# Kernel optimization log

Measured on AMD Instinct MI355X. Metric: run time of the kernel, lower is better.

## Reference

```python
import jax, jax.numpy as jnp
import numpy as np
from jax import lax

HEADS = 8
L, B, D, H, V, T = 128, 16, 512, 512, 16000, 32


def setup_inputs() -> dict:
    key = jax.random.key(0)
    ks = jax.random.split(key, 16)
    p = lambda k, shape, fan: (jax.random.normal(k, shape, jnp.float32) * (fan ** -0.5))
    output_len = jnp.sort(jax.random.randint(ks[15], (B,), 1, T + 1))[::-1]
    output_len = output_len.at[0].set(T)  # max(output_len) == T, sorted descending
    return dict(
        memory=jax.random.normal(ks[0], (L, B, D), jnp.float32),
        emb=p(ks[1], (V, H), H),
        Wq=p(ks[2], (2 * H, H), 2 * H), bq=jnp.zeros((H,), jnp.float32),
        Wk=p(ks[3], (D, H), D), bk=jnp.zeros((H,), jnp.float32),
        Wv=p(ks[4], (D, H), D), bv=jnp.zeros((H,), jnp.float32),
        W_ih=p(ks[5], (H, 3 * H), H), b_ih=p(ks[6], (3 * H,), H),
        W_hh=p(ks[7], (H, 3 * H), H), b_hh=p(ks[8], (3 * H,), H),
        Wf=p(ks[9], (H, V), H), bf=jnp.zeros((V,), jnp.float32),
        output_len=output_len.astype(jnp.int32),
        max_output_len=T,
    )


def _forward(memory, emb, Wq, bq, Wk, bk, Wv, bv, W_ih, b_ih, W_hh, b_hh, Wf, bf,
             output_len, max_output_len):
    Lm, bs, _ = memory.shape
    Hh = emb.shape[1]
    dk = Hh // HEADS
    scale = 1.0 / np.sqrt(dk)

    def mha(query):  # query: (1, bs, 2H); recomputes k/v projections each step (faithful)
        qh = (query @ Wq + bq).reshape(1, bs, HEADS, dk).transpose(2, 1, 0, 3)   # (h,b,1,dk)
        kh = (memory @ Wk + bk).reshape(Lm, bs, HEADS, dk).transpose(2, 1, 0, 3)  # (h,b,L,dk)
        vh = (memory @ Wv + bv).reshape(Lm, bs, HEADS, dk).transpose(2, 1, 0, 3)
        score = jax.nn.softmax(jnp.einsum('hbqd,hbkd->hbqk', qh, kh) * scale, axis=-1)
        ctx = jnp.einsum('hbqk,hbkd->hbqd', score, vh)          # (h,b,1,dk)
        ctx = ctx.transpose(2, 1, 0, 3).reshape(1, bs, Hh)       # (1,b,H)
        sc = score.transpose(2, 1, 0, 3).mean(axis=2)            # (1,b,L) mean over heads
        return ctx, sc

    def gru_cell(x, h):  # (bs,H),(bs,H) -> (bs,H); PyTorch GRU equations
        gi = x @ W_ih + b_ih
        gh = h @ W_hh + b_hh
        ir, iz, inn = jnp.split(gi, 3, axis=-1)
        hr, hz, hn = jnp.split(gh, 3, axis=-1)
        r = jax.nn.sigmoid(ir + hr)
        z = jax.nn.sigmoid(iz + hz)
        n = jnp.tanh(inn + r * hn)
        return (1.0 - z) * n + z * h

    def step(carry, i):
        out, hid = carry  # (bs,V), (bs,H)
        embedded = emb[jnp.argmax(out, axis=-1)]                 # (bs,H)
        query = jnp.concatenate([embedded, hid], axis=-1)[None]  # (1,bs,2H)
        ctx, sc = mha(query)
        h_new = gru_cell(ctx[0], hid)
        logits = h_new @ Wf + bf                                 # fc on GRU output
        # masking replaces torch's shrinking-batch slicing (output_len sorted desc)
        active = (i < output_len)[:, None].astype(logits.dtype)
        return (logits, h_new), (logits * active, h_new * active, sc[0] * active)

    init = (jnp.zeros((bs, Wf.shape[1]), memory.dtype), jnp.zeros((bs, Hh), memory.dtype))
    _, (outputs, hiddens, scores) = lax.scan(step, init, jnp.arange(max_output_len))
    return outputs, hiddens, scores


def reference(memory, emb, Wq, bq, Wk, bk, Wv, bv, W_ih, b_ih, W_hh, b_hh, Wf, bf,
              output_len, max_output_len):
    return _forward(memory, emb, Wq, bq, Wk, bk, Wv, bv, W_ih, b_ih, W_hh, b_hh,
                    Wf, bf, output_len, max_output_len)
```

## Files before the change

### kernel.cpp

```cpp
#include <hip/hip_runtime.h>

#define LL 128
#define BB 16
#define HH 512
#define VV 16000
#define TT 32
#define NH 8
#define DK 64

#define WS_K 0
#define WS_V (LL*BB*HH)
#define WS_HID0 (2*LL*BB*HH)
#define WS_HID1 (WS_HID0 + BB*HH)
#define WS_CTX  (WS_HID1 + BB*HH)
#define WS_P    (WS_CTX + BB*HH)
#define WS_HS   (WS_P + BB*NH*LL)
#define WS_SLOTS_F (WS_HS + 6*BB*HH)

#define OUT_HID_OFF ((size_t)TT*BB*VV)
#define OUT_SC_OFF  (OUT_HID_OFF + (size_t)TT*BB*HH)


__global__ __launch_bounds__(256) void kv_kernel(const float* __restrict__ mem,
        const float* __restrict__ Wk, const float* __restrict__ bk,
        const float* __restrict__ Wv, const float* __restrict__ bv,
        float* __restrict__ ws) {
    int blk = blockIdx.x;
    int rg = blk >> 4, ct = blk & 15;
    int isV = ct >= 8;
    int colbase = (ct & 7) * 64;
    const float* W = isV ? Wv : Wk;
    const float* bias = isV ? bv : bk;
    float* outp = ws + (isV ? WS_V : WS_K);
    int rowbase = rg * 16;
    int tid = threadIdx.x;
    __shared__ float As[16*516];

    {
        const float4* srcp = (const float4*)(mem + (size_t)rowbase*512);
        #pragma unroll
        for (int j = 0; j < 8; ++j) {
            int i = tid + 256*j;
            float4 v = srcp[i];
            int row = i >> 7, c4i = i & 127;
            *(float4*)(As + row*516 + c4i*4) = v;
        }
    }
    if (blk == 0) {
        for (int i = tid; i < BB*HH; i += 256) ws[WS_HID0 + i] = 0.f;
        unsigned long long* slots = (unsigned long long*)(ws + WS_SLOTS_F);
        for (int i = tid; i < (TT+1)*BB; i += 256)
            slots[i] = (i < BB) ? 0xFFFFFFFFull : 0ull;
    }
    __syncthreads();

    int cq = tid & 15;
    int rq4 = (tid >> 4) & 3;
    int kq = tid >> 6;
    float acc[4][4];
    #pragma unroll
    for (int i = 0; i < 4; ++i) { acc[i][0]=0.f; acc[i][1]=0.f; acc[i][2]=0.f; acc[i][3]=0.f; }
    const float* wp = W + colbase + cq*4;
    for (int k4 = kq*32; k4 < kq*32 + 32; ++k4) {
        float4 a0 = *(const float4*)(As + (rq4*4+0)*516 + k4*4);
        float4 a1 = *(const float4*)(As + (rq4*4+1)*516 + k4*4);
        float4 a2 = *(const float4*)(As + (rq4*4+2)*516 + k4*4);
        float4 a3 = *(const float4*)(As + (rq4*4+3)*516 + k4*4);
        const float* wrow = wp + (size_t)(4*k4)*512;
        float4 w0 = *(const float4*)(wrow);
        float4 w1 = *(const float4*)(wrow + 512);
        float4 w2 = *(const float4*)(wrow + 1024);
        float4 w3 = *(const float4*)(wrow + 1536);
        #define KV_FMA(ri, A) \
            acc[ri][0] += A.x*w0.x + A.y*w1.x + A.z*w2.x + A.w*w3.x; \
            acc[ri][1] += A.x*w0.y + A.y*w1.y + A.z*w2.y + A.w*w3.y; \
            acc[ri][2] += A.x*w0.z + A.y*w1.z + A.z*w2.z + A.w*w3.z; \
            acc[ri][3] += A.x*w0.w + A.y*w1.w + A.z*w2.w + A.w*w3.w;
        KV_FMA(0, a0) KV_FMA(1, a1) KV_FMA(2, a2) KV_FMA(3, a3)
        #undef KV_FMA
    }
    __syncthreads();
    float* red = As;
    #pragma unroll
    for (int ri = 0; ri < 4; ++ri)
        *(float4*)(red + ri*1024 + tid*4) =
            make_float4(acc[ri][0], acc[ri][1], acc[ri][2], acc[ri][3]);
    __syncthreads();
    {
        int c4 = tid & 15, row = tid >> 4;
        int rq = row >> 2, ri = row & 3;
        float4 b4v = *(const float4*)(bias + colbase + c4*4);
        float o[4] = {b4v.x, b4v.y, b4v.z, b4v.w};
        #pragma unroll
        for (int kq2 = 0; kq2 < 4; ++kq2) {
            const float* pr = red + ri*1024 + (kq2*64 + rq*16 + c4)*4;
            o[0] += pr[0]; o[1] += pr[1]; o[2] += pr[2]; o[3] += pr[3];
        }
        *(float4*)(outp + (size_t)(rowbase + row)*512 + colbase + c4*4) =
            make_float4(o[0], o[1], o[2], o[3]);
    }
}

__global__ __launch_bounds__(256) void attn_kernel(
        const float* __restrict__ emb, const float* __restrict__ Wq,
        const float* __restrict__ bq, float* __restrict__ ws, int t) {
    int b = blockIdx.x >> 3, h = blockIdx.x & 7;
    int tid = threadIdx.x;
    const float* hid = ws + ((t & 1) ? WS_HID1 : WS_HID0);
    unsigned long long* slots = (unsigned long long*)(ws + WS_SLOTS_F);
    __shared__ float q[2*HH];
    __shared__ float part[8*64];
    __shared__ float qh[64];
    __shared__ float sp[2*LL];
    __shared__ float p[LL];
    __shared__ float cpart[4*64];

    unsigned long long slot = slots[t*BB + b];
    unsigned idx = 0xFFFFFFFFu - (unsigned)(slot & 0xFFFFFFFFull);
    for (int i = tid; i < HH; i += 256) {
        q[i] = emb[(size_t)idx*HH + i];
        q[HH + i] = hid[b*HH + i];
    }
    __syncthreads();

    {
        int c2 = tid & 31, kc = tid >> 5;
        const float* wp = Wq + (size_t)(kc*128)*HH + h*64 + c2*2;
        const float* qp = q + kc*128;
        float a0 = 0.f, a1 = 0.f;
        #pragma unroll 8
        for (int kk = 0; kk < 128; ++kk) {
            float x = qp[kk];
            float2 w2 = *(const float2*)(wp + (size_t)kk*HH);
            a0 += x*w2.x; a1 += x*w2.y;
        }
        part[kc*64 + c2*2]     = a0;
        part[kc*64 + c2*2 + 1] = a1;
    }
    __syncthreads();
    if (tid < 64) {
        float s = bq[h*64 + tid];
        #pragma unroll
        for (int kc = 0; kc < 8; ++kc) s += part[kc*64 + tid];
        qh[tid] = s;
    }
    __syncthreads();

    {
        int l = tid & 127, jh = tid >> 7;
        const float4* kr = (const float4*)(ws + WS_K + ((size_t)(l*BB + b))*HH + h*DK) + jh*8;
        const float4* q4 = (const float4*)qh + jh*8;
        float acc = 0.f;
        #pragma unroll
        for (int j = 0; j < 8; ++j) {
            float4 kv = kr[j], qq = q4[j];
            acc += qq.x*kv.x + qq.y*kv.y + qq.z*kv.z + qq.w*kv.w;
        }
        sp[jh*128 + l] = acc;
    }
    __syncthreads();

    if (tid < 64) {
        float s0 = (sp[tid]      + sp[128 + tid]) * 0.125f;
        float s1 = (sp[64 + tid] + sp[192 + tid]) * 0.125f;
        float m = fmaxf(s0, s1);
        #pragma unroll
        for (int off = 32; off; off >>= 1) m = fmaxf(m, __shfl_xor(m, off));
        float e0 = expf(s0 - m), e1 = expf(s1 - m);
        float sum = e0 + e1;
        #pragma unroll
        for (int off = 32; off; off >>= 1) sum += __shfl_xor(sum, off);
        float inv = 1.f / sum;
        p[tid]      = e0 * inv;
        p[64 + tid] = e1 * inv;
    }
    __syncthreads();
    if (tid < 128) ws[WS_P + (size_t)(b*NH + h)*LL + tid] = p[tid];

    {
        int c = tid & 63, lc = tid >> 6;
        const float* Vp = ws + WS_V + h*DK + c;
        float acc = 0.f;
        #pragma unroll 8
        for (int li = 0; li < 32; ++li) {
            int l = lc*32 + li;
            acc += p[l] * Vp[(size_t)(l*BB + b)*HH];
        }
        cpart[lc*64 + c] = acc;
    }
    __syncthreads();
    if (tid < 64)
        ws[WS_CTX + b*HH + h*DK + tid] =
            cpart[tid] + cpart[64+tid] + cpart[128+tid] + cpart[192+tid];
}

__global__ __launch_bounds__(512) void gates_kernel(
        const float* __restrict__ Wih, const float* __restrict__ bih,
        const float* __restrict__ Whh, const float* __restrict__ bhh,
        const int* __restrict__ olen, float* __restrict__ ws,
        float* __restrict__ out, int t) {
    int cb = blockIdx.x;
    int tid = threadIdx.x;
    const float* hid_in = ws + ((t & 1) ? WS_HID1 : WS_HID0);
    float* hid_out = ws + ((t & 1) ? WS_HID0 : WS_HID1);
    const float* ctx = ws + WS_CTX;
    __shared__ float xs[512*20];
    __shared__ float hh[512*20];
    __shared__ float part[8*256];
    __shared__ float gacc[6*256];

    for (int i = tid; i < BB*HH; i += 512) {
        int bb = i >> 9, k = i & 511;
        xs[k*20 + bb] = ctx[i];
        hh[k*20 + bb] = hid_in[i];
    }
    if (tid < 64) {
        int e = cb*64 + tid;
        int b = e >> 7, l = e & 127;
        float s = 0.f;
        #pragma unroll
        for (int hq = 0; hq < NH; ++hq)
            s += ws[WS_P + (size_t)(b*NH + hq)*LL + l];
        out[OUT_SC_OFF + ((size_t)t*BB + b)*LL + l] = (t < olen[b]) ? s*0.125f : 0.f;
    }
    __syncthreads();

    int c4 = tid & 3, b4 = (tid >> 2) & 3, kc = tid >> 4;
    int wv = tid >> 6;
    for (int g = 0; g < 6; ++g) {
        const float* W = (g < 3) ? Wih : Whh;
        int gg = (g < 3) ? g : g - 3;
        const float* xsrc = (g < 3) ? xs : hh;
        const float* wp = W + (size_t)kc*(3*HH) + gg*HH + cb*16 + c4*4;
        const float* xp = xsrc + kc*20 + b4*4;
        float acc[4][4];
        #pragma unroll
        for (int i = 0; i < 4; ++i) { acc[i][0]=0.f; acc[i][1]=0.f; acc[i][2]=0.f; acc[i][3]=0.f; }
        #pragma unroll 8
        for (int i = 0; i < 16; ++i) {
            float4 w4 = *(const float4*)wp;
            float4 x4 = *(const float4*)xp;
            wp += (size_t)32*(3*HH);
            xp += 32*20;
            acc[0][0] += x4.x*w4.x; acc[0][1] += x4.x*w4.y; acc[0][2] += x4.x*w4.z; acc[0][3] += x4.x*w4.w;
            acc[1][0] += x4.y*w4.x; acc[1][1] += x4.y*w4.y; acc[1][2] += x4.y*w4.z; acc[1][3] += x4.y*w4.w;
            acc[2][0] += x4.z*w4.x; acc[2][1] += x4.z*w4.y; acc[2][2] += x4.z*w4.z; acc[2][3] += x4.z*w4.w;
            acc[3][0] += x4.w*w4.x; acc[3][1] += x4.w*w4.y; acc[3][2] += x4.w*w4.z; acc[3][3] += x4.w*w4.w;
        }
        #pragma unroll
        for (int bi = 0; bi < 4; ++bi)
            #pragma unroll
            for (int ci = 0; ci < 4; ++ci) {
                float v = acc[bi][ci];
                v += __shfl_xor(v, 16);
                v += __shfl_xor(v, 32);
                acc[bi][ci] = v;
            }
        if ((tid & 48) == 0) {
            #pragma unroll
            for (int bi = 0; bi < 4; ++bi)
                *(float4*)(part + wv*256 + (b4*4+bi)*16 + c4*4) =
                    make_float4(acc[bi][0], acc[bi][1], acc[bi][2], acc[bi][3]);
        }
        __syncthreads();
        if (tid < 256) {
            int b = tid >> 4, c = tid & 15;
            float s = 0.f;
            #pragma unroll
            for (int w = 0; w < 8; ++w) s += part[w*256 + b*16 + c];
            gacc[g*256 + b*16 + c] = s;
        }
        __syncthreads();
    }

    if (tid < 256) {
        int b = tid >> 4, c = tid & 15;
        int col = cb*16 + c;
        float gir = gacc[0*256 + b*16 + c] + bih[col];
        float giz = gacc[1*256 + b*16 + c] + bih[HH + col];
        float gin = gacc[2*256 + b*16 + c] + bih[2*HH + col];
        float ghr = gacc[3*256 + b*16 + c] + bhh[col];
        float ghz = gacc[4*256 + b*16 + c] + bhh[HH + col];
        float ghn = gacc[5*256 + b*16 + c] + bhh[2*HH + col];
        float r = 1.f/(1.f + __expf(-(gir + ghr)));
        float z = 1.f/(1.f + __expf(-(giz + ghz)));
        float xn = gin + r*ghn;
        float n = 1.f - 2.f/(__expf(2.f*xn) + 1.f);
        float hprev = hh[col*20 + b];
        float hnew = (1.f - z)*n + z*hprev;
        hid_out[b*HH + col] = hnew;
        out[OUT_HID_OFF + ((size_t)t*BB + b)*HH + col] = (t < olen[b]) ? hnew : 0.f;
        ws[WS_HS + col*16 + b] = hnew;
    }
}

__global__ __launch_bounds__(256) void logits_kernel(
        const float* __restrict__ Wf, const float* __restrict__ bf,
        const int* __restrict__ olen, float* __restrict__ ws,
        float* __restrict__ out, int t) {
    __shared__ float hs[HH*20];
    __shared__ float red[4*512];
    __shared__ unsigned long long am[BB*16];
    int tid = threadIdx.x;

    {
        const float4* s4 = (const float4*)(ws + WS_HS);
        #pragma unroll
        for (int j = 0; j < 8; ++j) {
            int i = tid + 256*j;
            float4 v = s4[i];
            int row = i >> 2, qo = i & 3;
            *(float4*)(hs + row*20 + qo*4) = v;
        }
    }
    __syncthreads();

    int c4 = tid & 7, kc = tid >> 3;
    int colbase = blockIdx.x * 32;
    float acc[16][4];
    #pragma unroll
    for (int bi = 0; bi < 16; ++bi) { acc[bi][0]=0.f; acc[bi][1]=0.f; acc[bi][2]=0.f; acc[bi][3]=0.f; }
    const float* wp = Wf + (size_t)kc*VV + colbase + c4*4;
    const float* hp = hs + kc*20;
    #pragma unroll 8
    for (int i = 0; i < 16; ++i) {
        float4 w4 = *(const float4*)wp;
        float4 h0 = *(const float4*)(hp);
        float4 h1 = *(const float4*)(hp + 4);
        float4 h2 = *(const float4*)(hp + 8);
        float4 h3 = *(const float4*)(hp + 12);
        wp += (size_t)32 * VV;
        hp += 32 * 20;
        #define LACC(bi, hv) acc[bi][0] += (hv)*w4.x; acc[bi][1] += (hv)*w4.y; \
                             acc[bi][2] += (hv)*w4.z; acc[bi][3] += (hv)*w4.w;
        LACC(0,h0.x)  LACC(1,h0.y)  LACC(2,h0.z)  LACC(3,h0.w)
        LACC(4,h1.x)  LACC(5,h1.y)  LACC(6,h1.z)  LACC(7,h1.w)
        LACC(8,h2.x)  LACC(9,h2.y)  LACC(10,h2.z) LACC(11,h2.w)
        LACC(12,h3.x) LACC(13,h3.y) LACC(14,h3.z) LACC(15,h3.w)
        #undef LACC
    }

    #pragma unroll
    for (int bi = 0; bi < 16; ++bi)
        #pragma unroll
        for (int ci = 0; ci < 4; ++ci) {
            float v = acc[bi][ci];
            v += __shfl_xor(v, 8);
            v += __shfl_xor(v, 16);
            v += __shfl_xor(v, 32);
            acc[bi][ci] = v;
        }
    int wv = tid >> 6;
    if ((tid & 56) == 0) {
        #pragma unroll
        for (int bi = 0; bi < 16; ++bi)
            *(float4*)(red + wv*512 + bi*32 + c4*4) =
                make_float4(acc[bi][0], acc[bi][1], acc[bi][2], acc[bi][3]);
    }
    __syncthreads();

    {
        int b = tid >> 4, cp = (tid & 15) * 2;
        float2 bf2 = *(const float2*)(bf + colbase + cp);
        float v0 = bf2.x, v1 = bf2.y;
        #pragma unroll
        for (int w = 0; w < 4; ++w) {
            v0 += red[w*512 + b*32 + cp];
            v1 += red[w*512 + b*32 + cp + 1];
        }
        bool active = t < olen[b];
        float2 ov; ov.x = active ? v0 : 0.f; ov.y = active ? v1 : 0.f;
        *(float2*)(out + ((size_t)t*BB + b)*VV + colbase + cp) = ov;

        unsigned u0 = __float_as_uint(v0);
        u0 = (u0 & 0x80000000u) ? ~u0 : (u0 | 0x80000000u);
        unsigned u1 = __float_as_uint(v1);
        u1 = (u1 & 0x80000000u) ? ~u1 : (u1 | 0x80000000u);
        unsigned long long e0 = ((unsigned long long)u0 << 32)
                              | (unsigned long long)(0xFFFFFFFFu - (unsigned)(colbase + cp));
        unsigned long long e1 = ((unsigned long long)u1 << 32)
                              | (unsigned long long)(0xFFFFFFFFu - (unsigned)(colbase + cp + 1));
        am[b*16 + (tid & 15)] = e0 > e1 ? e0 : e1;
    }
    __syncthreads();
    if (tid < BB) {
        unsigned long long m = 0ull;
        #pragma unroll
        for (int i = 0; i < 16; ++i) {
            unsigned long long v = am[tid*16 + i];
            m = v > m ? v : m;
        }
        unsigned long long* slots = (unsigned long long*)(ws + WS_SLOTS_F);
        atomicMax(&slots[(size_t)(t+1)*BB + tid], m);
    }
}

extern "C" void kernel_launch(void* const* d_in, const int* in_sizes, int n_in,
                              void* d_out, int out_size, void* d_ws, size_t ws_size,
                              hipStream_t stream) {
    const float* mem = (const float*)d_in[0];
    const float* emb = (const float*)d_in[1];
    const float* Wq  = (const float*)d_in[2];
    const float* bq  = (const float*)d_in[3];
    const float* Wk  = (const float*)d_in[4];
    const float* bk  = (const float*)d_in[5];
    const float* Wv  = (const float*)d_in[6];
    const float* bv  = (const float*)d_in[7];
    const float* Wih = (const float*)d_in[8];
    const float* bih = (const float*)d_in[9];
    const float* Whh = (const float*)d_in[10];
    const float* bhh = (const float*)d_in[11];
    const float* Wf  = (const float*)d_in[12];
    const float* bf  = (const float*)d_in[13];
    const int* olen  = (const int*)d_in[14];
    float* out = (float*)d_out;
    float* ws  = (float*)d_ws;

    hipLaunchKernelGGL(kv_kernel, dim3(2048), dim3(256), 0, stream, mem, Wk, bk, Wv, bv, ws);
    for (int t = 0; t < TT; ++t) {
        hipLaunchKernelGGL(attn_kernel, dim3(BB*NH), dim3(256), 0, stream, emb, Wq, bq, ws, t);
        hipLaunchKernelGGL(gates_kernel, dim3(32), dim3(512), 0, stream,
                           Wih, bih, Whh, bhh, olen, ws, out, t);
        hipLaunchKernelGGL(logits_kernel, dim3(500), dim3(256), 0, stream,
                           Wf, bf, olen, ws, out, t);
    }
}
```

Measured before the change: 1.463 ms.

## Fuse per-step kernels into persistent mega kernel with software grid barriers

Replaces the 96 per-timestep launches of the attention, gate and logits kernels with one persistent kernel of 250 blocks of 512 threads. The stages are separated by an atomic sense-reversing grid barrier, which removes launch overhead and inter-kernel gaps. Hidden state and context are kept in transposed layout so the GRU can read the hidden state directly from global memory. Each stage is re-tiled for 512 threads, and logits now use 64 columns per block across 250 blocks. The cost is that stages run on fewer blocks, and correctness relies on all 250 blocks being co-resident, with deadlock possible otherwise.

```diff
diff --git a/kernel.cpp b/kernel.cpp
--- a/kernel.cpp
+++ b/kernel.cpp
@@ -7,15 +7,16 @@
 #define TT 32
 #define NH 8
 #define DK 64
+#define NBLK 250
 
 #define WS_K 0
 #define WS_V (LL*BB*HH)
-#define WS_HID0 (2*LL*BB*HH)
-#define WS_HID1 (WS_HID0 + BB*HH)
-#define WS_CTX  (WS_HID1 + BB*HH)
-#define WS_P    (WS_CTX + BB*HH)
-#define WS_HS   (WS_P + BB*NH*LL)
-#define WS_SLOTS_F (WS_HS + 6*BB*HH)
+#define WS_CTXT (2*LL*BB*HH)
+#define WS_HS0 (WS_CTXT + BB*HH)
+#define WS_HS1 (WS_HS0 + BB*HH)
+#define WS_P   (WS_HS1 + BB*HH)
+#define WS_SLOTS_F (WS_P + BB*NH*LL)
+#define WS_BAR (WS_SLOTS_F + 2*(TT+1)*BB + 16)
 
 #define OUT_HID_OFF ((size_t)TT*BB*VV)
 #define OUT_SC_OFF  (OUT_HID_OFF + (size_t)TT*BB*HH)
@@ -47,10 +48,11 @@
         }
     }
     if (blk == 0) {
-        for (int i = tid; i < BB*HH; i += 256) ws[WS_HID0 + i] = 0.f;
+        for (int i = tid; i < BB*HH; i += 256) ws[WS_HS0 + i] = 0.f;
         unsigned long long* slots = (unsigned long long*)(ws + WS_SLOTS_F);
         for (int i = tid; i < (TT+1)*BB; i += 256)
             slots[i] = (i < BB) ? 0xFFFFFFFFull : 0ull;
+        if (tid == 0) *(unsigned*)(ws + WS_BAR) = 0u;
     }
     __syncthreads();
 
@@ -101,297 +103,345 @@
     }
 }
 
-__global__ __launch_bounds__(256) void attn_kernel(
+__device__ __forceinline__ void gridbar(unsigned* cnt, unsigned* sense,
+                                        unsigned target) {
+    __syncthreads();
+    if (threadIdx.x == 0) {
+        __threadfence();
+        unsigned old = atomicAdd(cnt, 1u);
+        if (old == (unsigned)NBLK - 1u) {
+            __hip_atomic_store(cnt, 0u, __ATOMIC_RELAXED, __HIP_MEMORY_SCOPE_AGENT);
+            __hip_atomic_fetch_add(sense, 1u, __ATOMIC_RELEASE, __HIP_MEMORY_SCOPE_AGENT);
+        } else {
+            while ((int)(__hip_atomic_load(sense, __ATOMIC_RELAXED,
+                         __HIP_MEMORY_SCOPE_AGENT) - target) < 0)
+                __builtin_amdgcn_s_sleep(8);
+        }
+        __threadfence();
+    }
+    __syncthreads();
+}
+
+__global__ __launch_bounds__(512) void mega_kernel(
         const float* __restrict__ emb, const float* __restrict__ Wq,
-        const float* __restrict__ bq, float* __restrict__ ws, int t) {
-    int b = blockIdx.x >> 3, h = blockIdx.x & 7;
-    int tid = threadIdx.x;
-    const float* hid = ws + ((t & 1) ? WS_HID1 : WS_HID0);
-    unsigned long long* slots = (unsigned long long*)(ws + WS_SLOTS_F);
-    __shared__ float q[2*HH];
-    __shared__ float part[8*64];
-    __shared__ float qh[64];
-    __shared__ float sp[2*LL];
-    __shared__ float p[LL];
-    __shared__ float cpart[4*64];
-
-    unsigned long long slot = slots[t*BB + b];
-    unsigned idx = 0xFFFFFFFFu - (unsigned)(slot & 0xFFFFFFFFull);
-    for (int i = tid; i < HH; i += 256) {
-        q[i] = emb[(size_t)idx*HH + i];
-        q[HH + i] = hid[b*HH + i];
-    }
-    __syncthreads();
-
-    {
-        int c2 = tid & 31, kc = tid >> 5;
-        const float* wp = Wq + (size_t)(kc*128)*HH + h*64 + c2*2;
-        const float* qp = q + kc*128;
-        float a0 = 0.f, a1 = 0.f;
-        #pragma unroll 8
-        for (int kk = 0; kk < 128; ++kk) {
-            float x = qp[kk];
-            float2 w2 = *(const float2*)(wp + (size_t)kk*HH);
-            a0 += x*w2.x; a1 += x*w2.y;
-        }
-        part[kc*64 + c2*2]     = a0;
-        part[kc*64 + c2*2 + 1] = a1;
-    }
-    __syncthreads();
-    if (tid < 64) {
-        float s = bq[h*64 + tid];
-        #pragma unroll
-        for (int kc = 0; kc < 8; ++kc) s += part[kc*64 + tid];
-        qh[tid] = s;
-    }
-    __syncthreads();
-
-    {
-        int l = tid & 127, jh = tid >> 7;
-        const float4* kr = (const float4*)(ws + WS_K + ((size_t)(l*BB + b))*HH + h*DK) + jh*8;
-        const float4* q4 = (const float4*)qh + jh*8;
-        float acc = 0.f;
-        #pragma unroll
-        for (int j = 0; j < 8; ++j) {
-            float4 kv = kr[j], qq = q4[j];
-            acc += qq.x*kv.x + qq.y*kv.y + qq.z*kv.z + qq.w*kv.w;
-        }
-        sp[jh*128 + l] = acc;
-    }
-    __syncthreads();
-
-    if (tid < 64) {
-        float s0 = (sp[tid]      + sp[128 + tid]) * 0.125f;
-        float s1 = (sp[64 + tid] + sp[192 + tid]) * 0.125f;
-        float m = fmaxf(s0, s1);
-        #pragma unroll
-        for (int off = 32; off; off >>= 1) m = fmaxf(m, __shfl_xor(m, off));
-        float e0 = expf(s0 - m), e1 = expf(s1 - m);
-        float sum = e0 + e1;
-        #pragma unroll
-        for (int off = 32; off; off >>= 1) sum += __shfl_xor(sum, off);
-        float inv = 1.f / sum;
-        p[tid]      = e0 * inv;
-        p[64 + tid] = e1 * inv;
-    }
-    __syncthreads();
-    if (tid < 128) ws[WS_P + (size_t)(b*NH + h)*LL + tid] = p[tid];
-
-    {
-        int c = tid & 63, lc = tid >> 6;
-        const float* Vp = ws + WS_V + h*DK + c;
-        float acc = 0.f;
-        #pragma unroll 8
-        for (int li = 0; li < 32; ++li) {
-            int l = lc*32 + li;
-            acc += p[l] * Vp[(size_t)(l*BB + b)*HH];
-        }
-        cpart[lc*64 + c] = acc;
-    }
-    __syncthreads();
-    if (tid < 64)
-        ws[WS_CTX + b*HH + h*DK + tid] =
-            cpart[tid] + cpart[64+tid] + cpart[128+tid] + cpart[192+tid];
-}
-
-__global__ __launch_bounds__(512) void gates_kernel(
+        const float* __restrict__ bq,
         const float* __restrict__ Wih, const float* __restrict__ bih,
         const float* __restrict__ Whh, const float* __restrict__ bhh,
+        const float* __restrict__ Wf,  const float* __restrict__ bf,
         const int* __restrict__ olen, float* __restrict__ ws,
-        float* __restrict__ out, int t) {
-    int cb = blockIdx.x;
-    int tid = threadIdx.x;
-    const float* hid_in = ws + ((t & 1) ? WS_HID1 : WS_HID0);
-    float* hid_out = ws + ((t & 1) ? WS_HID0 : WS_HID1);
-    const float* ctx = ws + WS_CTX;
-    __shared__ float xs[512*20];
-    __shared__ float hh[512*20];
-    __shared__ float part[8*256];
-    __shared__ float gacc[6*256];
-
-    for (int i = tid; i < BB*HH; i += 512) {
-        int bb = i >> 9, k = i & 511;
-        xs[k*20 + bb] = ctx[i];
-        hh[k*20 + bb] = hid_in[i];
-    }
-    if (tid < 64) {
-        int e = cb*64 + tid;
-        int b = e >> 7, l = e & 127;
-        float s = 0.f;
-        #pragma unroll
-        for (int hq = 0; hq < NH; ++hq)
-            s += ws[WS_P + (size_t)(b*NH + hq)*LL + l];
-        out[OUT_SC_OFF + ((size_t)t*BB + b)*LL + l] = (t < olen[b]) ? s*0.125f : 0.f;
-    }
-    __syncthreads();
-
-    int c4 = tid & 3, b4 = (tid >> 2) & 3, kc = tid >> 4;
-    int wv = tid >> 6;
-    for (int g = 0; g < 6; ++g) {
-        const float* W = (g < 3) ? Wih : Whh;
-        int gg = (g < 3) ? g : g - 3;
-        const float* xsrc = (g < 3) ? xs : hh;
-        const float* wp = W + (size_t)kc*(3*HH) + gg*HH + cb*16 + c4*4;
-        const float* xp = xsrc + kc*20 + b4*4;
-        float acc[4][4];
-        #pragma unroll
-        for (int i = 0; i < 4; ++i) { acc[i][0]=0.f; acc[i][1]=0.f; acc[i][2]=0.f; acc[i][3]=0.f; }
-        #pragma unroll 8
-        for (int i = 0; i < 16; ++i) {
-            float4 w4 = *(const float4*)wp;
-            float4 x4 = *(const float4*)xp;
-            wp += (size_t)32*(3*HH);
-            xp += 32*20;
-            acc[0][0] += x4.x*w4.x; acc[0][1] += x4.x*w4.y; acc[0][2] += x4.x*w4.z; acc[0][3] += x4.x*w4.w;
-            acc[1][0] += x4.y*w4.x; acc[1][1] += x4.y*w4.y; acc[1][2] += x4.y*w4.z; acc[1][3] += x4.y*w4.w;
-            acc[2][0] += x4.z*w4.x; acc[2][1] += x4.z*w4.y; acc[2][2] += x4.z*w4.z; acc[2][3] += x4.z*w4.w;
-            acc[3][0] += x4.w*w4.x; acc[3][1] += x4.w*w4.y; acc[3][2] += x4.w*w4.z; acc[3][3] += x4.w*w4.w;
-        }
-        #pragma unroll
-        for (int bi = 0; bi < 4; ++bi)
+        float* __restrict__ out) {
+    __shared__ __align__(16) char s_raw[57344];
+    int blk = blockIdx.x, tid = threadIdx.x;
+    unsigned* cnt = (unsigned*)(ws + WS_BAR);
+    unsigned* sense = cnt + 1;
+    unsigned s0 = 0;
+    if (tid == 0)
+        s0 = __hip_atomic_load(sense, __ATOMIC_ACQUIRE, __HIP_MEMORY_SCOPE_AGENT);
+    unsigned bno = 0;
+    unsigned long long* slots = (unsigned long long*)(ws + WS_SLOTS_F);
+
+    for (int t = 0; t < TT; ++t) {
+        const float* hs_prev = ws + ((t & 1) ? WS_HS1 : WS_HS0);
+        float* hs_new = ws + ((t & 1) ? WS_HS0 : WS_HS1);
+
+        if (blk < 128) {
+            int b = blk >> 3, h = blk & 7;
+            float* q     = (float*)s_raw;
+            float* part  = q + 1024;
+            float* qh    = part + 1024;
+            float* sp    = qh + 64;
+            float* p     = sp + 512;
+            float* cpart = p + 128;
+
+            unsigned long long slot = slots[t*BB + b];
+            unsigned idx = 0xFFFFFFFFu - (unsigned)(slot & 0xFFFFFFFFull);
+            q[tid] = emb[(size_t)idx*HH + tid];
+            q[HH + tid] = hs_prev[tid*16 + b];
+            __syncthreads();
+
+            {
+                int c2 = tid & 31, kc = tid >> 5;
+                const float* wp = Wq + (size_t)(kc*64)*HH + h*64 + c2*2;
+                const float* qp = q + kc*64;
+                float a0 = 0.f, a1 = 0.f;
+                #pragma unroll 8
+                for (int kk = 0; kk < 64; ++kk) {
+                    float x = qp[kk];
+                    float2 w2 = *(const float2*)(wp + (size_t)kk*HH);
+                    a0 += x*w2.x; a1 += x*w2.y;
+                }
+                part[kc*64 + c2*2]     = a0;
+                part[kc*64 + c2*2 + 1] = a1;
+            }
+            __syncthreads();
+            if (tid < 64) {
+                float s = bq[h*64 + tid];
+                #pragma unroll
+                for (int kc = 0; kc < 16; ++kc) s += part[kc*64 + tid];
+                qh[tid] = s;
+            }
+            __syncthreads();
+
+            {
+                int l = tid & 127, jh = tid >> 7;
+                const float4* kr = (const float4*)(ws + WS_K +
+                                   ((size_t)(l*BB + b))*HH + h*DK) + jh*4;
+                const float4* q4 = (const float4*)qh + jh*4;
+                float acc = 0.f;
+                #pragma unroll
+                for (int j = 0; j < 4; ++j) {
+                    float4 kv = kr[j], qq = q4[j];
+                    acc += qq.x*kv.x + qq.y*kv.y + qq.z*kv.z + qq.w*kv.w;
+                }
+                sp[jh*128 + l] = acc;
+            }
+            __syncthreads();
+
+            if (tid < 64) {
+                float s0v = (sp[tid]    + sp[128+tid]    + sp[256+tid]    + sp[384+tid])    * 0.125f;
+                float s1v = (sp[64+tid] + sp[128+64+tid] + sp[256+64+tid] + sp[384+64+tid]) * 0.125f;
+                float m = fmaxf(s0v, s1v);
+                #pragma unroll
+                for (int off = 32; off; off >>= 1) m = fmaxf(m, __shfl_xor(m, off));
+                float e0 = __expf(s0v - m), e1 = __expf(s1v - m);
+                float sum = e0 + e1;
+                #pragma unroll
+                for (int off = 32; off; off >>= 1) sum += __shfl_xor(sum, off);
+                float inv = 1.f / sum;
+                p[tid]      = e0 * inv;
+                p[64 + tid] = e1 * inv;
+            }
+            __syncthreads();
+            if (tid < 128) ws[WS_P + (size_t)(b*NH + h)*LL + tid] = p[tid];
+
+            {
+                int c = tid & 63, lc = tid >> 6;
+                const float* Vp = ws + WS_V + h*DK + c;
+                float acc = 0.f;
+                #pragma unroll 8
+                for (int li = 0; li < 16; ++li) {
+                    int l = lc*16 + li;
+                    acc += p[l] * Vp[(size_t)(l*BB + b)*HH];
+                }
+                cpart[lc*64 + c] = acc;
+            }
+            __syncthreads();
+            if (tid < 64) {
+                float v = cpart[tid];
+                #pragma unroll
+                for (int lc = 1; lc < 8; ++lc) v += cpart[lc*64 + tid];
+                ws[WS_CTXT + (size_t)(h*64 + tid)*16 + b] = v;
+            }
+        }
+        ++bno; gridbar(cnt, sense, s0 + bno);
+
+        if (blk < 32) {
+            int cb = blk;
+            float* xs   = (float*)s_raw;
+            float* part = xs + 512*20;
+            float* gacc = part + 8*256;
+
+            {
+                const float4* s4 = (const float4*)(ws + WS_CTXT);
+                #pragma unroll
+                for (int j = 0; j < 4; ++j) {
+                    int i = tid + 512*j;
+                    float4 v = s4[i];
+                    int k = i >> 2, qo = i & 3;
+                    *(float4*)(xs + k*20 + qo*4) = v;
+                }
+            }
+            if (tid < 64) {
+                int e = cb*64 + tid;
+                int b = e >> 7, l = e & 127;
+                float s = 0.f;
+                #pragma unroll
+                for (int hq = 0; hq < NH; ++hq)
+                    s += ws[WS_P + (size_t)(b*NH + hq)*LL + l];
+                out[OUT_SC_OFF + ((size_t)t*BB + b)*LL + l] =
+                    (t < olen[b]) ? s*0.125f : 0.f;
+            }
+            __syncthreads();
+
+            int c4 = tid & 3, b4 = (tid >> 2) & 3, kc = tid >> 4;
+            int wv = tid >> 6;
+            for (int g = 0; g < 6; ++g) {
+                const float* W = (g < 3) ? Wih : Whh;
+                int gg = (g < 3) ? g : g - 3;
+                const float* wp = W + (size_t)kc*(3*HH) + gg*HH + cb*16 + c4*4;
+                float acc[4][4];
+                #pragma unroll
+                for (int i = 0; i < 4; ++i) { acc[i][0]=0.f; acc[i][1]=0.f; acc[i][2]=0.f; acc[i][3]=0.f; }
+                if (g < 3) {
+                    const float* xp = xs + kc*20 + b4*4;
+                    #pragma unroll 8
+                    for (int i = 0; i < 16; ++i) {
+                        float4 w4 = *(const float4*)wp;
+                        float4 x4 = *(const float4*)xp;
+                        wp += (size_t)32*(3*HH);
+                        xp += 32*20;
+                        acc[0][0] += x4.x*w4.x; acc[0][1] += x4.x*w4.y; acc[0][2] += x4.x*w4.z; acc[0][3] += x4.x*w4.w;
+                        acc[1][0] += x4.y*w4.x; acc[1][1] += x4.y*w4.y; acc[1][2] += x4.y*w4.z; acc[1][3] += x4.y*w4.w;
+                        acc[2][0] += x4.z*w4.x; acc[2][1] += x4.z*w4.y; acc[2][2] += x4.z*w4.z; acc[2][3] += x4.z*w4.w;
+                        acc[3][0] += x4.w*w4.x; acc[3][1] += x4.w*w4.y; acc[3][2] += x4.w*w4.z; acc[3][3] += x4.w*w4.w;
+                    }
+                } else {
+                    const float* xp = hs_prev + kc*16 + b4*4;
+                    #pragma unroll 8
+                    for (int i = 0; i < 16; ++i) {
+                        float4 w4 = *(const float4*)wp;
+                        float4 x4 = *(const float4*)xp;
+                        wp += (size_t)32*(3*HH);
+                        xp += 32*16;
+                        acc[0][0] += x4.x*w4.x; acc[0][1] += x4.x*w4.y; acc[0][2] += x4.x*w4.z; acc[0][3] += x4.x*w4.w;
+                        acc[1][0] += x4.y*w4.x; acc[1][1] += x4.y*w4.y; acc[1][2] += x4.y*w4.z; acc[1][3] += x4.y*w4.w;
+                        acc[2][0] += x4.z*w4.x; acc[2][1] += x4.z*w4.y; acc[2][2] += x4.z*w4.z; acc[2][3] += x4.z*w4.w;
+                        acc[3][0] += x4.w*w4.x; acc[3][1] += x4.w*w4.y; acc[3][2] += x4.w*w4.z; acc[3][3] += x4.w*w4.w;
+                    }
+                }
+                #pragma unroll
+                for (int bi = 0; bi < 4; ++bi)
+                    #pragma unroll
+                    for (int ci = 0; ci < 4; ++ci) {
+                        float v = acc[bi][ci];
+                        v += __shfl_xor(v, 16);
+                        v += __shfl_xor(v, 32);
+                        acc[bi][ci] = v;
+                    }
+                if ((tid & 48) == 0) {
+                    #pragma unroll
+                    for (int bi = 0; bi < 4; ++bi)
+                        *(float4*)(part + wv*256 + (b4*4+bi)*16 + c4*4) =
+                            make_float4(acc[bi][0], acc[bi][1], acc[bi][2], acc[bi][3]);
+                }
+                __syncthreads();
+                if (tid < 256) {
+                    int b = tid >> 4, c = tid & 15;
+                    float s = 0.f;
+                    #pragma unroll
+                    for (int w = 0; w < 8; ++w) s += part[w*256 + b*16 + c];
+                    gacc[g*256 + b*16 + c] = s;
+                }
+                __syncthreads();
+            }
+
+            if (tid < 256) {
+                int b = tid >> 4, c = tid & 15;
+                int col = cb*16 + c;
+                float gir = gacc[0*256 + b*16 + c] + bih[col];
+                float giz = gacc[1*256 + b*16 + c] + bih[HH + col];
+                float gin = gacc[2*256 + b*16 + c] + bih[2*HH + col];
+                float ghr = gacc[3*256 + b*16 + c] + bhh[col];
+                float ghz = gacc[4*256 + b*16 + c] + bhh[HH + col];
+                float ghn = gacc[5*256 + b*16 + c] + bhh[2*HH + col];
+                float r = 1.f/(1.f + __expf(-(gir + ghr)));
+                float z = 1.f/(1.f + __expf(-(giz + ghz)));
+                float xn = gin + r*ghn;
+                float n = 1.f - 2.f/(__expf(2.f*xn) + 1.f);
+                float hprev = hs_prev[col*16 + b];
+                float hnew = (1.f - z)*n + z*hprev;
+                hs_new[col*16 + b] = hnew;
+                out[OUT_HID_OFF + ((size_t)t*BB + b)*HH + col] =
+                    (t < olen[b]) ? hnew : 0.f;
+            }
+        }
+        ++bno; gridbar(cnt, sense, s0 + bno);
+
+        {
+            float* hs = (float*)s_raw;
+            unsigned long long* am = (unsigned long long*)(s_raw + 40960);
+            int colbase = blk * 64;
+
+            {
+                const float4* s4 = (const float4*)hs_new;
+                #pragma unroll
+                for (int j = 0; j < 4; ++j) {
+                    int i = tid + 512*j;
+                    float4 v = s4[i];
+                    int k = i >> 2, qo = i & 3;
+                    *(float4*)(hs + k*20 + qo*4) = v;
+                }
+            }
+            __syncthreads();
+
+            int c4 = tid & 15, kc = tid >> 4;
+            float acc[16][4];
             #pragma unroll
-            for (int ci = 0; ci < 4; ++ci) {
-                float v = acc[bi][ci];
-                v += __shfl_xor(v, 16);
-                v += __shfl_xor(v, 32);
-                acc[bi][ci] = v;
-            }
-        if ((tid & 48) == 0) {
+            for (int bi = 0; bi < 16; ++bi) { acc[bi][0]=0.f; acc[bi][1]=0.f; acc[bi][2]=0.f; acc[bi][3]=0.f; }
+            const float* wp = Wf + (size_t)kc*VV + colbase + c4*4;
+            const float* hp = hs + kc*20;
+            #pragma unroll 8
+            for (int i = 0; i < 16; ++i) {
+                float4 w4 = *(const float4*)wp;
+                float4 h0 = *(const float4*)(hp);
+                float4 h1 = *(const float4*)(hp + 4);
+                float4 h2 = *(const float4*)(hp + 8);
+                float4 h3 = *(const float4*)(hp + 12);
+                wp += (size_t)32 * VV;
+                hp += 32 * 20;
+                #define LACC(bi, hv) acc[bi][0] += (hv)*w4.x; acc[bi][1] += (hv)*w4.y; \
+                                     acc[bi][2] += (hv)*w4.z; acc[bi][3] += (hv)*w4.w;
+                LACC(0,h0.x)  LACC(1,h0.y)  LACC(2,h0.z)  LACC(3,h0.w)
+                LACC(4,h1.x)  LACC(5,h1.y)  LACC(6,h1.z)  LACC(7,h1.w)
+                LACC(8,h2.x)  LACC(9,h2.y)  LACC(10,h2.z) LACC(11,h2.w)
+                LACC(12,h3.x) LACC(13,h3.y) LACC(14,h3.z) LACC(15,h3.w)
+                #undef LACC
+            }
             #pragma unroll
-            for (int bi = 0; bi < 4; ++bi)
-                *(float4*)(part + wv*256 + (b4*4+bi)*16 + c4*4) =
-                    make_float4(acc[bi][0], acc[bi][1], acc[bi][2], acc[bi][3]);
-        }
-        __syncthreads();
-        if (tid < 256) {
-            int b = tid >> 4, c = tid & 15;
-            float s = 0.f;
-            #pragma unroll
-            for (int w = 0; w < 8; ++w) s += part[w*256 + b*16 + c];
-            gacc[g*256 + b*16 + c] = s;
-        }
-        __syncthreads();
-    }
-
-    if (tid < 256) {
-        int b = tid >> 4, c = tid & 15;
-        int col = cb*16 + c;
-        float gir = gacc[0*256 + b*16 + c] + bih[col];
-        float giz = gacc[1*256 + b*16 + c] + bih[HH + col];
-        float gin = gacc[2*256 + b*16 + c] + bih[2*HH + col];
-        float ghr = gacc[3*256 + b*16 + c] + bhh[col];
-        float ghz = gacc[4*256 + b*16 + c] + bhh[HH + col];
-        float ghn = gacc[5*256 + b*16 + c] + bhh[2*HH + col];
-        float r = 1.f/(1.f + __expf(-(gir + ghr)));
-        float z = 1.f/(1.f + __expf(-(giz + ghz)));
-        float xn = gin + r*ghn;
-        float n = 1.f - 2.f/(__expf(2.f*xn) + 1.f);
-        float hprev = hh[col*20 + b];
-        float hnew = (1.f - z)*n + z*hprev;
-        hid_out[b*HH + col] = hnew;
-        out[OUT_HID_OFF + ((size_t)t*BB + b)*HH + col] = (t < olen[b]) ? hnew : 0.f;
-        ws[WS_HS + col*16 + b] = hnew;
-    }
-}
-
-__global__ __launch_bounds__(256) void logits_kernel(
-        const float* __restrict__ Wf, const float* __restrict__ bf,
-        const int* __restrict__ olen, float* __restrict__ ws,
-        float* __restrict__ out, int t) {
-    __shared__ float hs[HH*20];
-    __shared__ float red[4*512];
-    __shared__ unsigned long long am[BB*16];
-    int tid = threadIdx.x;
-
-    {
-        const float4* s4 = (const float4*)(ws + WS_HS);
-        #pragma unroll
-        for (int j = 0; j < 8; ++j) {
-            int i = tid + 256*j;
-            float4 v = s4[i];
-            int row = i >> 2, qo = i & 3;
-            *(float4*)(hs + row*20 + qo*4) = v;
-        }
-    }
-    __syncthreads();
-
-    int c4 = tid & 7, kc = tid >> 3;
-    int colbase = blockIdx.x * 32;
-    float acc[16][4];
-    #pragma unroll
-    for (int bi = 0; bi < 16; ++bi) { acc[bi][0]=0.f; acc[bi][1]=0.f; acc[bi][2]=0.f; acc[bi][3]=0.f; }
-    const float* wp = Wf + (size_t)kc*VV + colbase + c4*4;
-    const float* hp = hs + kc*20;
-    #pragma unroll 8
-    for (int i = 0; i < 16; ++i) {
-        float4 w4 = *(const float4*)wp;
-        float4 h0 = *(const float4*)(hp);
-        float4 h1 = *(const float4*)(hp + 4);
-        float4 h2 = *(const float4*)(hp + 8);
-        float4 h3 = *(const float4*)(hp + 12);
-        wp += (size_t)32 * VV;
-        hp += 32 * 20;
-        #define LACC(bi, hv) acc[bi][0] += (hv)*w4.x; acc[bi][1] += (hv)*w4.y; \
-                             acc[bi][2] += (hv)*w4.z; acc[bi][3] += (hv)*w4.w;
-        LACC(0,h0.x)  LACC(1,h0.y)  LACC(2,h0.z)  LACC(3,h0.w)
-        LACC(4,h1.x)  LACC(5,h1.y)  LACC(6,h1.z)  LACC(7,h1.w)
-        LACC(8,h2.x)  LACC(9,h2.y)  LACC(10,h2.z) LACC(11,h2.w)
-        LACC(12,h3.x) LACC(13,h3.y) LACC(14,h3.z) LACC(15,h3.w)
-        #undef LACC
-    }
-
-    #pragma unroll
-    for (int bi = 0; bi < 16; ++bi)
-        #pragma unroll
-        for (int ci = 0; ci < 4; ++ci) {
-            float v = acc[bi][ci];
-            v += __shfl_xor(v, 8);
-            v += __shfl_xor(v, 16);
-            v += __shfl_xor(v, 32);
-            acc[bi][ci] = v;
-        }
-    int wv = tid >> 6;
-    if ((tid & 56) == 0) {
-        #pragma unroll
-        for (int bi = 0; bi < 16; ++bi)
-            *(float4*)(red + wv*512 + bi*32 + c4*4) =
-                make_float4(acc[bi][0], acc[bi][1], acc[bi][2], acc[bi][3]);
-    }
-    __syncthreads();
-
-    {
-        int b = tid >> 4, cp = (tid & 15) * 2;
-        float2 bf2 = *(const float2*)(bf + colbase + cp);
-        float v0 = bf2.x, v1 = bf2.y;
-        #pragma unroll
-        for (int w = 0; w < 4; ++w) {
-            v0 += red[w*512 + b*32 + cp];
-            v1 += red[w*512 + b*32 + cp + 1];
-        }
-        bool active = t < olen[b];
-        float2 ov; ov.x = active ? v0 : 0.f; ov.y = active ? v1 : 0.f;
-        *(float2*)(out + ((size_t)t*BB + b)*VV + colbase + cp) = ov;
-
-        unsigned u0 = __float_as_uint(v0);
-        u0 = (u0 & 0x80000000u) ? ~u0 : (u0 | 0x80000000u);
-        unsigned u1 = __float_as_uint(v1);
-        u1 = (u1 & 0x80000000u) ? ~u1 : (u1 | 0x80000000u);
-        unsigned long long e0 = ((unsigned long long)u0 << 32)
-                              | (unsigned long long)(0xFFFFFFFFu - (unsigned)(colbase + cp));
-        unsigned long long e1 = ((unsigned long long)u1 << 32)
-                              | (unsigned long long)(0xFFFFFFFFu - (unsigned)(colbase + cp + 1));
-        am[b*16 + (tid & 15)] = e0 > e1 ? e0 : e1;
-    }
-    __syncthreads();
-    if (tid < BB) {
-        unsigned long long m = 0ull;
-        #pragma unroll
-        for (int i = 0; i < 16; ++i) {
-            unsigned long long v = am[tid*16 + i];
-            m = v > m ? v : m;
-        }
-        unsigned long long* slots = (unsigned long long*)(ws + WS_SLOTS_F);
-        atomicMax(&slots[(size_t)(t+1)*BB + tid], m);
+            for (int bi = 0; bi < 16; ++bi)
+                #pragma unroll
+                for (int ci = 0; ci < 4; ++ci) {
+                    float v = acc[bi][ci];
+                    v += __shfl_xor(v, 16);
+                    v += __shfl_xor(v, 32);
+                    acc[bi][ci] = v;
+                }
+            __syncthreads();
+            float* red = (float*)s_raw;
+            int wv = tid >> 6;
+            if ((tid & 48) == 0) {
+                #pragma unroll
+                for (int bi = 0; bi < 16; ++bi)
+                    *(float4*)(red + wv*1024 + bi*64 + c4*4) =
+                        make_float4(acc[bi][0], acc[bi][1], acc[bi][2], acc[bi][3]);
+            }
+            __syncthreads();
+
+            {
+                int b = tid >> 5, cp = (tid & 31) * 2;
+                float2 bf2 = *(const float2*)(bf + colbase + cp);
+                float v0 = bf2.x, v1 = bf2.y;
+                #pragma unroll
+                for (int w = 0; w < 8; ++w) {
+                    v0 += red[w*1024 + b*64 + cp];
+                    v1 += red[w*1024 + b*64 + cp + 1];
+                }
+                bool active = t < olen[b];
+                float2 ov; ov.x = active ? v0 : 0.f; ov.y = active ? v1 : 0.f;
+                *(float2*)(out + ((size_t)t*BB + b)*VV + colbase + cp) = ov;
+
+                unsigned u0 = __float_as_uint(v0);
+                u0 = (u0 & 0x80000000u) ? ~u0 : (u0 | 0x80000000u);
+                unsigned u1 = __float_as_uint(v1);
+                u1 = (u1 & 0x80000000u) ? ~u1 : (u1 | 0x80000000u);
+                unsigned long long e0 = ((unsigned long long)u0 << 32)
+                    | (unsigned long long)(0xFFFFFFFFu - (unsigned)(colbase + cp));
+                unsigned long long e1 = ((unsigned long long)u1 << 32)
+                    | (unsigned long long)(0xFFFFFFFFu - (unsigned)(colbase + cp + 1));
+                am[b*32 + (tid & 31)] = e0 > e1 ? e0 : e1;
+            }
+            __syncthreads();
+            if (tid < BB) {
+                unsigned long long m = 0ull;
+                #pragma unroll
+                for (int i = 0; i < 32; ++i) {
+                    unsigned long long v = am[tid*32 + i];
+                    m = v > m ? v : m;
+                }
+                atomicMax(&slots[(size_t)(t+1)*BB + tid], m);
+            }
+        }
+        if (t < TT - 1) { ++bno; gridbar(cnt, sense, s0 + bno); }
     }
 }
 
@@ -417,11 +467,6 @@
     float* ws  = (float*)d_ws;
 
     hipLaunchKernelGGL(kv_kernel, dim3(2048), dim3(256), 0, stream, mem, Wk, bk, Wv, bv, ws);
-    for (int t = 0; t < TT; ++t) {
-        hipLaunchKernelGGL(attn_kernel, dim3(BB*NH), dim3(256), 0, stream, emb, Wq, bq, ws, t);
-        hipLaunchKernelGGL(gates_kernel, dim3(32), dim3(512), 0, stream,
-                           Wih, bih, Whh, bhh, olen, ws, out, t);
-        hipLaunchKernelGGL(logits_kernel, dim3(500), dim3(256), 0, stream,
-                           Wf, bf, olen, ws, out, t);
-    }
+    hipLaunchKernelGGL(mega_kernel, dim3(NBLK), dim3(512), 0, stream,
+                       emb, Wq, bq, Wih, bih, Whh, bhh, Wf, bf, olen, ws, out);
 }
```

Result: slower. 3.372 ms (+130.4%).
